# Performance work log

Hardware: AMD Instinct MI355X
Metric: run time of the kernel (lower is better)

The kernel has to match this reference:

```python
import jax, jax.numpy as jnp
import numpy as np

B, S, D_IN, D, H = 2, 2048, 1024, 1024, 16
HD = D // H

def setup_inputs() -> dict:
    key = jax.random.key(0)
    k1, k2, k3 = jax.random.split(key, 3)
    # xavier_uniform-style scale for weights
    lim_qkv = float(np.sqrt(6.0 / (D_IN + 3 * D)))
    lim_o = float(np.sqrt(6.0 / (D + D)))
    return {
        "x": jax.random.normal(k1, (B, S, D_IN), dtype=jnp.float32),
        "w_qkv": jax.random.uniform(k2, (3 * D, D_IN), dtype=jnp.float32, minval=-lim_qkv, maxval=lim_qkv),
        "b_qkv": jnp.zeros((3 * D,), dtype=jnp.float32),
        "w_o": jax.random.uniform(k3, (D, D), dtype=jnp.float32, minval=-lim_o, maxval=lim_o),
        "b_o": jnp.zeros((D,), dtype=jnp.float32),
    }

def reference(x, w_qkv, b_qkv, w_o, b_o):
    b, s, _ = x.shape
    # QKV projection: [B,S,3D]
    qkv = jnp.einsum("bsd,ed->bse", x, w_qkv) + b_qkv
    # [B,S,H,3*HD] -> [B,H,S,3*HD]
    qkv = qkv.reshape(b, s, H, 3 * HD).transpose(0, 2, 1, 3)
    q, k, v = jnp.split(qkv, 3, axis=-1)  # each [B,H,S,HD]
    scale = 1.0 / jnp.sqrt(jnp.asarray(HD, dtype=q.dtype))
    logits = jnp.einsum("bhqd,bhkd->bhqk", q, k) * scale  # [B,H,S,S]
    attn = jax.nn.softmax(logits, axis=-1)
    vals = jnp.einsum("bhqk,bhkd->bhqd", attn, v)  # [B,H,S,HD]
    vals = vals.transpose(0, 2, 1, 3).reshape(b, s, D)
    return jnp.einsum("bsd,ed->bse", vals, w_o) + b_o
```

## Files before the change

### kernel.cpp

```cpp
#include <hip/hip_runtime.h>
#include <hip/hip_bf16.h>
#include <math.h>

#define BATCH 2
#define SLEN  2048
#define DIN   1024
#define DMODEL 1024
#define NHEAD 16
#define HD    64
#define E3    3072

typedef unsigned short us;
typedef _Float16 f16;
typedef __attribute__((ext_vector_type(8))) _Float16 f16x8;
typedef __attribute__((ext_vector_type(8))) unsigned short us8;
typedef __attribute__((ext_vector_type(4))) unsigned short us4;
typedef __attribute__((ext_vector_type(4))) float f32x4;
typedef __attribute__((ext_vector_type(16))) float f32x16;

#define QSCALE 0.18033688011112042f

__device__ __forceinline__ us f16bits(float x) {
    const f16 h = (f16)x;
    return __builtin_bit_cast(us, h);
}

#define GLL16(g, l)                                                                     \
    __builtin_amdgcn_global_load_lds((const __attribute__((address_space(1))) unsigned int*)(g), \
                                     (__attribute__((address_space(3))) unsigned int*)(l), 16, 0, 0)

__global__ __launch_bounds__(256) void cvt3_f16(
    const float* __restrict__ x, us* __restrict__ ox, int nx,
    const float* __restrict__ wq, us* __restrict__ owq, int nq,
    const float* __restrict__ wo, us* __restrict__ owo)
{
    int i = (blockIdx.x * 256 + threadIdx.x) * 8;
    const float* s;
    us* o;
    if (i < nx)           { s = x;  o = ox; }
    else if (i < nx + nq) { s = wq; o = owq; i -= nx; }
    else                  { s = wo; o = owo; i -= nx + nq; }
    const float4 f0 = *(const float4*)&s[i];
    const float4 f1 = *(const float4*)&s[i + 4];
    const float v[8] = {f0.x, f0.y, f0.z, f0.w, f1.x, f1.y, f1.z, f1.w};
    us8 h;
#pragma unroll
    for (int j = 0; j < 8; ++j) h[j] = f16bits(v[j]);
    *(us8*)&o[i] = h;
}

template <bool QKV_OUT>
__global__ __launch_bounds__(256) void gemm_f16(
    const us* __restrict__ Am, const us* __restrict__ Bm,
    const float* __restrict__ bias, void* __restrict__ Cout,
    int M, int N, int K)
{
    __shared__ __align__(16) us As[128 * 32];
    __shared__ __align__(16) us Bs[128 * 32];

    const int t    = threadIdx.x;
    const int lane = t & 63;
    const int w    = t >> 6;
    const int ml   = lane & 15;
    const int quad = lane >> 4;
    const int wm   = w >> 1;
    const int wn   = w & 1;

    const int m0 = blockIdx.y * 128;
    const int n0 = blockIdx.x * 128;

    const int srow = (lane >> 2);
    const int scol = (lane & 3) * 8;

    const us* pA = Am + (size_t)(m0 + w * 32 + srow) * K + scol;
    const us* pB = Bm + (size_t)(n0 + w * 32 + srow) * K + scol;
    const size_t rstep = (size_t)16 * K;

    us* lA0 = &As[(w * 32) * 32];
    us* lA1 = &As[(w * 32 + 16) * 32];
    us* lB0 = &Bs[(w * 32) * 32];
    us* lB1 = &Bs[(w * 32 + 16) * 32];

    f32x4 acc[4][4];
#pragma unroll
    for (int i = 0; i < 4; ++i)
#pragma unroll
        for (int j = 0; j < 4; ++j) {
            acc[i][j][0] = 0.f; acc[i][j][1] = 0.f; acc[i][j][2] = 0.f; acc[i][j][3] = 0.f;
        }

    for (int k0 = 0; k0 < K; k0 += 32) {
        __syncthreads();
        GLL16(pA + k0, lA0); GLL16(pA + k0 + rstep, lA1);
        GLL16(pB + k0, lB0); GLL16(pB + k0 + rstep, lB1);
        __syncthreads();

        f16x8 a[4];
#pragma unroll
        for (int i = 0; i < 4; ++i)
            a[i] = __builtin_bit_cast(f16x8, *(const us8*)&As[(wm * 64 + i * 16 + ml) * 32 + quad * 8]);
#pragma unroll
        for (int j = 0; j < 4; ++j) {
            const f16x8 b = __builtin_bit_cast(f16x8, *(const us8*)&Bs[(wn * 64 + j * 16 + ml) * 32 + quad * 8]);
#pragma unroll
            for (int i = 0; i < 4; ++i)
                acc[i][j] = __builtin_amdgcn_mfma_f32_16x16x32_f16(a[i], b, acc[i][j], 0, 0, 0);
        }
    }

    float bj[4], cs[4];
#pragma unroll
    for (int j = 0; j < 4; ++j) {
        const int col = n0 + wn * 64 + j * 16 + ml;
        bj[j] = bias[col];
        cs[j] = (QKV_OUT && (col % 192) < 64) ? QSCALE : 1.0f;
    }

#pragma unroll
    for (int i = 0; i < 4; ++i) {
#pragma unroll
        for (int r = 0; r < 4; ++r) {
            const size_t rowoff = (size_t)(m0 + wm * 64 + i * 16 + quad * 4 + r) * N;
#pragma unroll
            for (int j = 0; j < 4; ++j) {
                const int col = n0 + wn * 64 + j * 16 + ml;
                const float v = (acc[i][j][r] + bj[j]) * cs[j];
                if (QKV_OUT) ((us*)Cout)[rowoff + col] = f16bits(v);
                else         ((float*)Cout)[rowoff + col] = v;
            }
        }
    }
}

#define ABQ 128
#define ACH 64
#define NCH (SLEN / ACH)
#define LQA 72

__global__ __launch_bounds__(256) void attn_mfma(
    const us* __restrict__ qkvh, us* __restrict__ vals)
{
    __shared__ __align__(16) us QPs[ABQ * LQA];
    __shared__ __align__(16) us Ks[ACH * LQA];
    __shared__ __align__(16) us Vt[HD * LQA];

    const int t    = threadIdx.x;
    const int lane = t & 63;
    const int w    = t >> 6;
    const int m32  = lane & 31;
    const int half = lane >> 5;

    const int bh = blockIdx.y;
    const int b  = bh >> 4;
    const int h  = bh & 15;
    const int q0 = blockIdx.x * ABQ;

    const size_t base = (size_t)b * SLEN * E3;
    const int qoff = h * 192;

    {
        const int row = t >> 1;
        const int c0  = (t & 1) * 32;
        const us* g = &qkvh[base + (size_t)(q0 + row) * E3 + qoff + c0];
#pragma unroll
        for (int s = 0; s < 4; ++s)
            *(us8*)&QPs[row * LQA + c0 + s * 8] = *(const us8*)(g + s * 8);
    }
    __syncthreads();

    f16x8 aq[4];
#pragma unroll
    for (int s = 0; s < 4; ++s)
        aq[s] = __builtin_bit_cast(f16x8, *(const us8*)&QPs[(w * 32 + m32) * LQA + half * 8 + 16 * s]);

    const int krA = t >> 2;
    const int ksA = (t & 3) * 16;
    const int krB = t & 63;
    const int ksB = w * 16;

    us8 kk0, kk1, vv0, vv1;
    {
        const us* gK = &qkvh[base + (size_t)(krA) * E3 + qoff + 64 + ksA];
        kk0 = *(const us8*)gK; kk1 = *(const us8*)(gK + 8);
        const us* gV = &qkvh[base + (size_t)(krB) * E3 + qoff + 128 + ksB];
        vv0 = *(const us8*)gV; vv1 = *(const us8*)(gV + 8);
    }

    f32x16 O[2];
#pragma unroll
    for (int dt = 0; dt < 2; ++dt)
#pragma unroll
        for (int r = 0; r < 16; ++r) O[dt][r] = 0.f;
    float lpart = 0.f;

    const int prow = (w * 32 + m32) * LQA;

    for (int c = 0; c < NCH; ++c) {
        __syncthreads();
        *(us8*)&Ks[krA * LQA + ksA]     = kk0;
        *(us8*)&Ks[krA * LQA + ksA + 8] = kk1;
#pragma unroll
        for (int j = 0; j < 8; ++j) Vt[(ksB + j) * LQA + krB]     = vv0[j];
#pragma unroll
        for (int j = 0; j < 8; ++j) Vt[(ksB + 8 + j) * LQA + krB] = vv1[j];
        __syncthreads();
        if (c + 1 < NCH) {
            const us* gK = &qkvh[base + (size_t)((c + 1) * ACH + krA) * E3 + qoff + 64 + ksA];
            kk0 = *(const us8*)gK; kk1 = *(const us8*)(gK + 8);
            const us* gV = &qkvh[base + (size_t)((c + 1) * ACH + krB) * E3 + qoff + 128 + ksB];
            vv0 = *(const us8*)gV; vv1 = *(const us8*)(gV + 8);
        }

#pragma unroll
        for (int kt = 0; kt < 2; ++kt) {
            f32x16 z;
#pragma unroll
            for (int r = 0; r < 16; ++r) z[r] = 0.f;
#pragma unroll
            for (int s = 0; s < 4; ++s) {
                const f16x8 ak = __builtin_bit_cast(f16x8, *(const us8*)&Ks[(kt * 32 + m32) * LQA + half * 8 + 16 * s]);
                z = __builtin_amdgcn_mfma_f32_32x32x16_f16(ak, aq[s], z, 0, 0, 0);
            }
#pragma unroll
            for (int g = 0; g < 4; ++g) {
                us4 pp;
#pragma unroll
                for (int r2 = 0; r2 < 4; ++r2) {
                    const float p = __builtin_amdgcn_exp2f(z[g * 4 + r2]);
                    lpart += p;
                    pp[r2] = f16bits(p);
                }
                *(us4*)&QPs[prow + kt * 32 + 8 * g + 4 * half] = pp;
            }
        }

        f16x8 pf[4];
#pragma unroll
        for (int s = 0; s < 4; ++s)
            pf[s] = __builtin_bit_cast(f16x8, *(const us8*)&QPs[prow + half * 8 + 16 * s]);
#pragma unroll
        for (int dt = 0; dt < 2; ++dt) {
#pragma unroll
            for (int s = 0; s < 4; ++s) {
                const f16x8 av = __builtin_bit_cast(f16x8, *(const us8*)&Vt[(dt * 32 + m32) * LQA + half * 8 + 16 * s]);
                O[dt] = __builtin_amdgcn_mfma_f32_32x32x16_f16(av, pf[s], O[dt], 0, 0, 0);
            }
        }
    }

    const float l  = lpart + __shfl_xor(lpart, 32);
    const float rl = 1.0f / l;
    const int sq = q0 + w * 32 + m32;
    const size_t rowbase = (size_t)(b * SLEN + sq) * DMODEL + h * HD;
#pragma unroll
    for (int dt = 0; dt < 2; ++dt) {
#pragma unroll
        for (int g = 0; g < 4; ++g) {
            us4 o4;
#pragma unroll
            for (int r2 = 0; r2 < 4; ++r2) o4[r2] = f16bits(O[dt][g * 4 + r2] * rl);
            *(us4*)&vals[rowbase + dt * 32 + 8 * g + 4 * half] = o4;
        }
    }
}

extern "C" void kernel_launch(void* const* d_in, const int* in_sizes, int n_in,
                              void* d_out, int out_size, void* d_ws, size_t ws_size,
                              hipStream_t stream) {
    const float* x     = (const float*)d_in[0];
    const float* w_qkv = (const float*)d_in[1];
    const float* b_qkv = (const float*)d_in[2];
    const float* w_o   = (const float*)d_in[3];
    const float* b_o   = (const float*)d_in[4];
    float* out = (float*)d_out;

    const int M   = BATCH * SLEN;
    const int XN  = M * DIN;
    const int WQN = E3 * DIN;
    const int WON = DMODEL * DMODEL;
    const size_t QKVN = (size_t)BATCH * SLEN * E3;

    us* qkvh = (us*)d_ws;
    us* xh   = qkvh + QKVN;
    us* wq   = xh + XN;
    us* wo   = wq + WQN;

    cvt3_f16<<<dim3((XN + WQN + WON) / 2048), 256, 0, stream>>>(
        x, xh, XN, w_qkv, wq, WQN, w_o, wo);

    gemm_f16<true><<<dim3(E3 / 128, M / 128), 256, 0, stream>>>(
        xh, wq, b_qkv, qkvh, M, E3, DIN);

    us* vals = xh;
    attn_mfma<<<dim3(SLEN / ABQ, BATCH * NHEAD), 256, 0, stream>>>(qkvh, vals);

    gemm_f16<false><<<dim3(DMODEL / 128, M / 128), 256, 0, stream>>>(
        vals, wo, b_o, out, M, DMODEL, DMODEL);
}
```

Measured before the change: 201.0 us.

## Split attention KV range across two warp groups and keep P in registers

Doubles the attention block to 512 threads, with two groups of four waves each processing half of the key chunks. The partial outputs and row sums are merged through shared memory at the end. The P matrix is now built in registers with packed round-toward-zero conversion and permlane32 swaps, removing the LDS round-trip for P. V is transposed using 32-bit packed stores. This adds parallelism per block and cuts shared-memory traffic, at the cost of a merge step, higher LDS use and a different rounding mode for P.

```diff
diff --git a/kernel.cpp b/kernel.cpp
--- a/kernel.cpp
+++ b/kernel.cpp
@@ -13,16 +13,26 @@
 typedef unsigned short us;
 typedef _Float16 f16;
 typedef __attribute__((ext_vector_type(8))) _Float16 f16x8;
+typedef __attribute__((ext_vector_type(2))) _Float16 f16x2;
 typedef __attribute__((ext_vector_type(8))) unsigned short us8;
 typedef __attribute__((ext_vector_type(4))) unsigned short us4;
 typedef __attribute__((ext_vector_type(4))) float f32x4;
 typedef __attribute__((ext_vector_type(16))) float f32x16;
+typedef __attribute__((ext_vector_type(4))) unsigned int u32x4;
 
 #define QSCALE 0.18033688011112042f
 
 __device__ __forceinline__ us f16bits(float x) {
     const f16 h = (f16)x;
     return __builtin_bit_cast(us, h);
+}
+
+__device__ __forceinline__ unsigned int pkrtz(float a, float b) {
+    return __builtin_bit_cast(unsigned int, __builtin_amdgcn_cvt_pkrtz(a, b));
+}
+
+__device__ __forceinline__ void plswap(unsigned int& a, unsigned int& b) {
+    asm volatile("v_permlane32_swap_b32 %0, %1" : "+v"(a), "+v"(b));
 }
 
 #define GLL16(g, l)                                                                     \
@@ -135,18 +145,24 @@
 #define ABQ 128
 #define ACH 64
 #define NCH (SLEN / ACH)
+#define NCH2 (NCH / 2)
 #define LQA 72
-
-__global__ __launch_bounds__(256) void attn_mfma(
+#define OSTR 68
+
+__global__ __launch_bounds__(512, 4) void attn_mfma(
     const us* __restrict__ qkvh, us* __restrict__ vals)
 {
-    __shared__ __align__(16) us QPs[ABQ * LQA];
-    __shared__ __align__(16) us Ks[ACH * LQA];
-    __shared__ __align__(16) us Vt[HD * LQA];
+    __shared__ __align__(16) us smem[27648];
+    us* const Qs = smem;
+    us* const Ks = smem + 9216;
+    us* const Vt = smem + 18432;
 
     const int t    = threadIdx.x;
     const int lane = t & 63;
     const int w    = t >> 6;
+    const int sp   = w >> 2;
+    const int wq4  = w & 3;
+    const int t2   = t & 255;
     const int m32  = lane & 31;
     const int half = lane >> 5;
 
@@ -159,31 +175,34 @@
     const int qoff = h * 192;
 
     {
-        const int row = t >> 1;
-        const int c0  = (t & 1) * 32;
-        const us* g = &qkvh[base + (size_t)(q0 + row) * E3 + qoff + c0];
-#pragma unroll
-        for (int s = 0; s < 4; ++s)
-            *(us8*)&QPs[row * LQA + c0 + s * 8] = *(const us8*)(g + s * 8);
+        const int row = t >> 2;
+        const int c0q = (t & 3) * 16;
+        const us* g = &qkvh[base + (size_t)(q0 + row) * E3 + qoff + c0q];
+        *(us8*)&Qs[row * LQA + c0q]     = *(const us8*)g;
+        *(us8*)&Qs[row * LQA + c0q + 8] = *(const us8*)(g + 8);
     }
     __syncthreads();
 
     f16x8 aq[4];
 #pragma unroll
     for (int s = 0; s < 4; ++s)
-        aq[s] = __builtin_bit_cast(f16x8, *(const us8*)&QPs[(w * 32 + m32) * LQA + half * 8 + 16 * s]);
-
-    const int krA = t >> 2;
-    const int ksA = (t & 3) * 16;
-    const int krB = t & 63;
-    const int ksB = w * 16;
+        aq[s] = __builtin_bit_cast(f16x8, *(const us8*)&Qs[(wq4 * 32 + m32) * LQA + half * 8 + 16 * s]);
+
+    const int krA = t2 >> 2;
+    const int ksA = (t2 & 3) * 16;
+    const int k2  = t2 & 31;
+    const int d0v = (t2 >> 5) * 8;
+
+    us* const myK = Ks + sp * 4608;
+    us* const myV = Vt + sp * 4608;
+    const int cg0 = sp * NCH2;
 
     us8 kk0, kk1, vv0, vv1;
     {
-        const us* gK = &qkvh[base + (size_t)(krA) * E3 + qoff + 64 + ksA];
+        const us* gK = &qkvh[base + (size_t)(cg0 * ACH + krA) * E3 + qoff + 64 + ksA];
         kk0 = *(const us8*)gK; kk1 = *(const us8*)(gK + 8);
-        const us* gV = &qkvh[base + (size_t)(krB) * E3 + qoff + 128 + ksB];
-        vv0 = *(const us8*)gV; vv1 = *(const us8*)(gV + 8);
+        const us* gV = &qkvh[base + (size_t)(cg0 * ACH + 2 * k2) * E3 + qoff + 128 + d0v];
+        vv0 = *(const us8*)gV; vv1 = *(const us8*)(gV + E3);
     }
 
     f32x16 O[2];
@@ -193,24 +212,25 @@
         for (int r = 0; r < 16; ++r) O[dt][r] = 0.f;
     float lpart = 0.f;
 
-    const int prow = (w * 32 + m32) * LQA;
-
-    for (int c = 0; c < NCH; ++c) {
+    for (int c = 0; c < NCH2; ++c) {
         __syncthreads();
-        *(us8*)&Ks[krA * LQA + ksA]     = kk0;
-        *(us8*)&Ks[krA * LQA + ksA + 8] = kk1;
-#pragma unroll
-        for (int j = 0; j < 8; ++j) Vt[(ksB + j) * LQA + krB]     = vv0[j];
-#pragma unroll
-        for (int j = 0; j < 8; ++j) Vt[(ksB + 8 + j) * LQA + krB] = vv1[j];
+        *(us8*)&myK[krA * LQA + ksA]     = kk0;
+        *(us8*)&myK[krA * LQA + ksA + 8] = kk1;
+#pragma unroll
+        for (int j = 0; j < 8; ++j) {
+            const unsigned int pv = (unsigned int)vv0[j] | ((unsigned int)vv1[j] << 16);
+            *(unsigned int*)&myV[(d0v + j) * LQA + 2 * k2] = pv;
+        }
         __syncthreads();
-        if (c + 1 < NCH) {
-            const us* gK = &qkvh[base + (size_t)((c + 1) * ACH + krA) * E3 + qoff + 64 + ksA];
+        if (c + 1 < NCH2) {
+            const int cg = cg0 + c + 1;
+            const us* gK = &qkvh[base + (size_t)(cg * ACH + krA) * E3 + qoff + 64 + ksA];
             kk0 = *(const us8*)gK; kk1 = *(const us8*)(gK + 8);
-            const us* gV = &qkvh[base + (size_t)((c + 1) * ACH + krB) * E3 + qoff + 128 + ksB];
-            vv0 = *(const us8*)gV; vv1 = *(const us8*)(gV + 8);
-        }
-
+            const us* gV = &qkvh[base + (size_t)(cg * ACH + 2 * k2) * E3 + qoff + 128 + d0v];
+            vv0 = *(const us8*)gV; vv1 = *(const us8*)(gV + E3);
+        }
+
+        f16x8 pf[4];
 #pragma unroll
         for (int kt = 0; kt < 2; ++kt) {
             f32x16 z;
@@ -218,48 +238,69 @@
             for (int r = 0; r < 16; ++r) z[r] = 0.f;
 #pragma unroll
             for (int s = 0; s < 4; ++s) {
-                const f16x8 ak = __builtin_bit_cast(f16x8, *(const us8*)&Ks[(kt * 32 + m32) * LQA + half * 8 + 16 * s]);
+                const f16x8 ak = __builtin_bit_cast(f16x8, *(const us8*)&myK[(kt * 32 + m32) * LQA + half * 8 + 16 * s]);
                 z = __builtin_amdgcn_mfma_f32_32x32x16_f16(ak, aq[s], z, 0, 0, 0);
             }
+            float p[16];
+#pragma unroll
+            for (int r = 0; r < 16; ++r) {
+                p[r] = __builtin_amdgcn_exp2f(z[r]);
+                lpart += p[r];
+            }
+            unsigned int a0 = pkrtz(p[0],  p[1]),  a1 = pkrtz(p[2],  p[3]);
+            unsigned int b0 = pkrtz(p[4],  p[5]),  b1 = pkrtz(p[6],  p[7]);
+            plswap(a0, b0); plswap(a1, b1);
+            pf[2 * kt] = __builtin_bit_cast(f16x8, (u32x4){a0, a1, b0, b1});
+            unsigned int e0 = pkrtz(p[8],  p[9]),  e1 = pkrtz(p[10], p[11]);
+            unsigned int f0 = pkrtz(p[12], p[13]), f1 = pkrtz(p[14], p[15]);
+            plswap(e0, f0); plswap(e1, f1);
+            pf[2 * kt + 1] = __builtin_bit_cast(f16x8, (u32x4){e0, e1, f0, f1});
+        }
+
+#pragma unroll
+        for (int dt = 0; dt < 2; ++dt) {
+#pragma unroll
+            for (int s = 0; s < 4; ++s) {
+                const f16x8 av = __builtin_bit_cast(f16x8, *(const us8*)&myV[(dt * 32 + m32) * LQA + half * 8 + 16 * s]);
+                O[dt] = __builtin_amdgcn_mfma_f32_32x32x16_f16(av, pf[s], O[dt], 0, 0, 0);
+            }
+        }
+    }
+
+    const float l = lpart + __shfl_xor(lpart, 32);
+    const int ql = wq4 * 32 + m32;
+
+    __syncthreads();
+    float* const Osc = (float*)(smem + 9216);
+    float* const lsc = Osc + ABQ * OSTR;
+
+    if (sp == 1) {
+#pragma unroll
+        for (int dt = 0; dt < 2; ++dt) {
 #pragma unroll
             for (int g = 0; g < 4; ++g) {
-                us4 pp;
-#pragma unroll
-                for (int r2 = 0; r2 < 4; ++r2) {
-                    const float p = __builtin_amdgcn_exp2f(z[g * 4 + r2]);
-                    lpart += p;
-                    pp[r2] = f16bits(p);
-                }
-                *(us4*)&QPs[prow + kt * 32 + 8 * g + 4 * half] = pp;
-            }
-        }
-
-        f16x8 pf[4];
-#pragma unroll
-        for (int s = 0; s < 4; ++s)
-            pf[s] = __builtin_bit_cast(f16x8, *(const us8*)&QPs[prow + half * 8 + 16 * s]);
+                const f32x4 o4 = {O[dt][g * 4], O[dt][g * 4 + 1], O[dt][g * 4 + 2], O[dt][g * 4 + 3]};
+                *(f32x4*)&Osc[ql * OSTR + dt * 32 + 8 * g + 4 * half] = o4;
+            }
+        }
+        if (half == 0) lsc[ql] = l;
+    }
+    __syncthreads();
+    if (sp == 0) {
+        const float rl = 1.0f / (l + lsc[ql]);
+        const int sq = q0 + ql;
+        const size_t rowbase = (size_t)(b * SLEN + sq) * DMODEL + h * HD;
 #pragma unroll
         for (int dt = 0; dt < 2; ++dt) {
 #pragma unroll
-            for (int s = 0; s < 4; ++s) {
-                const f16x8 av = __builtin_bit_cast(f16x8, *(const us8*)&Vt[(dt * 32 + m32) * LQA + half * 8 + 16 * s]);
-                O[dt] = __builtin_amdgcn_mfma_f32_32x32x16_f16(av, pf[s], O[dt], 0, 0, 0);
-            }
-        }
-    }
-
-    const float l  = lpart + __shfl_xor(lpart, 32);
-    const float rl = 1.0f / l;
-    const int sq = q0 + w * 32 + m32;
-    const size_t rowbase = (size_t)(b * SLEN + sq) * DMODEL + h * HD;
-#pragma unroll
-    for (int dt = 0; dt < 2; ++dt) {
-#pragma unroll
-        for (int g = 0; g < 4; ++g) {
-            us4 o4;
-#pragma unroll
-            for (int r2 = 0; r2 < 4; ++r2) o4[r2] = f16bits(O[dt][g * 4 + r2] * rl);
-            *(us4*)&vals[rowbase + dt * 32 + 8 * g + 4 * half] = o4;
+            for (int g = 0; g < 4; ++g) {
+                const f32x4 part = *(const f32x4*)&Osc[ql * OSTR + dt * 32 + 8 * g + 4 * half];
+                us4 o4;
+#pragma unroll
+                for (int r2 = 0; r2 < 4; ++r2)
+                    o4[r2] = f16bits((O[dt][g * 4 + r2] + part[r2]) * rl);
+                *(us4*)&vals[rowbase + dt * 32 + 8 * g + 4 * half] = o4;
+            }
         }
     }
 }
@@ -292,7 +333,7 @@
         xh, wq, b_qkv, qkvh, M, E3, DIN);
 
     us* vals = xh;
-    attn_mfma<<<dim3(SLEN / ABQ, BATCH * NHEAD), 256, 0, stream>>>(qkvh, vals);
+    attn_mfma<<<dim3(SLEN / ABQ, BATCH * NHEAD), 512, 0, stream>>>(qkvh, vals);
 
     gemm_f16<false><<<dim3(DMODEL / 128, M / 128), 256, 0, stream>>>(
         vals, wo, b_o, out, M, DMODEL, DMODEL);
```

New measurement: 190.3 us. -5.4%, faster.
